# Kernel optimization log

Measured on AMD Instinct MI355X. Metric: run time of the kernel, lower is better.

The kernel has to match this reference:

```python
import jax, jax.numpy as jnp
import numpy as np

N = 16384   # total nodes (16 graphs x 32x32 grid)
E = 65536   # edges (before self loops)
F_IN = 7
H = 8       # gat heads
C = 200     # gat hidden per head
HC = H * C  # 1600
GCN = 1600
CNN = 64
OUT = 6
B = 16      # graphs per batch
G = 32      # grid size
EPS = 1e-5


def _bn1(x, g, b):
    # BatchNorm1d, training-mode batch stats (biased var), x: [N, F]
    mu = x.mean(0)
    var = x.var(0)
    return (x - mu) * jax.lax.rsqrt(var + EPS) * g + b


def _bn2(x, g, b):
    # BatchNorm2d over (N, H, W), x: [B, C, H, W]
    mu = x.mean((0, 2, 3), keepdims=True)
    var = x.var((0, 2, 3), keepdims=True)
    return (x - mu) * jax.lax.rsqrt(var + EPS) * g[None, :, None, None] + b[None, :, None, None]


def _conv5(x, w, b):
    y = jax.lax.conv_general_dilated(x, w, (1, 1), [(2, 2), (2, 2)],
                                     dimension_numbers=('NCHW', 'OIHW', 'NCHW'))
    return y + b[None, :, None, None]


def _gatv2(x, Wl, bl, Wr, br, We, att, bias, src, dst, edge_attr):
    # PyG GATv2Conv: concat=True, add_self_loops=True (fill_value='mean'), edge_dim=1
    n = x.shape[0]
    xl = (x @ Wl + bl).reshape(n, H, C)  # source transform
    xr = (x @ Wr + br).reshape(n, H, C)  # target transform
    loop = jnp.arange(n, dtype=src.dtype)
    s = jnp.concatenate([src, loop])
    d = jnp.concatenate([dst, loop])
    ea_loop = jnp.broadcast_to(edge_attr.mean(0, keepdims=True), (n, edge_attr.shape[1]))
    ea = jnp.concatenate([edge_attr, ea_loop], 0)
    ee = (ea @ We).reshape(-1, H, C)
    m = jax.nn.leaky_relu(xl[s] + xr[d] + ee, 0.2)       # [E+N, H, C]
    alpha = jnp.einsum('ehc,hc->eh', m, att)             # [E+N, H]
    amax = jax.ops.segment_max(alpha, d, num_segments=n)
    ex = jnp.exp(alpha - amax[d])
    denom = jax.ops.segment_sum(ex, d, num_segments=n)
    a = ex / denom[d]                                    # scatter-softmax over in-edges
    out = jax.ops.segment_sum(xl[s] * a[:, :, None], d, num_segments=n)  # [N, H, C]
    return out.reshape(n, HC) + bias


def setup_inputs() -> dict:
    k = jax.random.key(0)
    ks = jax.random.split(k, 16)
    def nrm(i, shape, s):
        return jax.random.normal(ks[i], shape, jnp.float32) * s
    z = lambda *s: jnp.zeros(s, jnp.float32)
    o = lambda *s: jnp.ones(s, jnp.float32)
    return {
        'x': nrm(0, (N, F_IN), 1.0),
        'edge_attr': jax.random.uniform(ks[1], (E, 1), jnp.float32),
        'Wl': nrm(2, (F_IN, HC), 0.3), 'bl': z(HC),
        'Wr': nrm(3, (F_IN, HC), 0.3), 'br': z(HC),
        'We': nrm(4, (1, HC), 0.3), 'att': nrm(5, (H, C), 0.1), 'gat_b': z(HC),
        'bn1_g': o(HC), 'bn1_b': z(HC),
        'W1': nrm(6, (HC, GCN), 0.025), 'b1': z(GCN),
        'bn2_g': o(GCN), 'bn2_b': z(GCN),
        'W2': nrm(7, (GCN, GCN), 0.025), 'b2': z(GCN),
        'Wp': nrm(8, (GCN, CNN), 0.025), 'bp': z(CNN),
        'cw1': nrm(9, (CNN, CNN, 5, 5), 0.025), 'cb1': z(CNN), 'g1': o(CNN), 'be1': z(CNN),
        'cw2': nrm(10, (128, CNN, 5, 5), 0.025), 'cb2': z(128), 'g2': o(128), 'be2': z(128),
        'cw3': nrm(11, (CNN, 128, 5, 5), 0.025), 'cb3': z(CNN), 'g3': o(CNN), 'be3': z(CNN),
        'cw4': nrm(12, (OUT, CNN, 5, 5), 0.025), 'cb4': z(OUT),
        'src': jax.random.randint(ks[13], (E,), 0, N, jnp.int32),
        'dst': jax.random.randint(ks[14], (E,), 0, N, jnp.int32),
    }


def reference(x, edge_attr, Wl, bl, Wr, br, We, att, gat_b, bn1_g, bn1_b,
              W1, b1, bn2_g, bn2_b, W2, b2, Wp, bp,
              cw1, cb1, g1, be1, cw2, cb2, g2, be2, cw3, cb3, g3, be3, cw4, cb4,
              src, dst):
    h = _gatv2(x, Wl, bl, Wr, br, We, att, gat_b, src, dst, edge_attr)
    h = jax.nn.leaky_relu(_bn1(h, bn1_g, bn1_b), 0.01)
    h = jax.nn.relu(_bn1(h @ W1 + b1, bn2_g, bn2_b))
    h = jax.nn.relu(h @ W2 + b2)
    # per-graph projection + reshape to grid (batch vector is contiguous arange//1024)
    h = (h @ Wp + bp).reshape(B, G, G, CNN).transpose(0, 3, 1, 2)  # [B, CNN, G, G]
    h = jax.nn.relu(_bn2(_conv5(h, cw1, cb1), g1, be1))
    h = jax.nn.relu(_bn2(_conv5(h, cw2, cb2), g2, be2))
    h = jax.nn.relu(_bn2(_conv5(h, cw3, cb3), g3, be3))
    return _conv5(h, cw4, cb4)  # [B, 6, G, G]
```

## Files before the change

kernel.cpp:

```cpp
#include <hip/hip_runtime.h>
#include <cstdint>
#include <cstddef>

#define N_NODES 16384
#define N_EDGES 65536
#define EN_TOT  (N_EDGES + N_NODES)
#define FIN 7
#define HC 1600
#define NH 8
#define CHD 200
#define GCN 1600
#define CNN 64
#define BATCH 16
#define BN_EPS 1e-5f

typedef unsigned short ushort_t;
typedef __attribute__((ext_vector_type(8))) short s8frag;
typedef __attribute__((ext_vector_type(4))) float f32x4;

__device__ __forceinline__ ushort_t f2bf(float f) {
    unsigned u = __float_as_uint(f);
    unsigned r = (u + 0x7FFFu + ((u >> 16) & 1u)) >> 16;
    return (ushort_t)r;
}
__device__ __forceinline__ float bf2f(ushort_t u) {
    return __uint_as_float(((unsigned)u) << 16);
}

__device__ __forceinline__ void gload16(const void* g, void* l) {
    __builtin_amdgcn_global_load_lds((const __attribute__((address_space(1))) void*)g,
                                     (__attribute__((address_space(3))) void*)l, 16, 0, 0);
}

#define SWZ_KOFF(tid) ((((tid) & 3) ^ (((tid) >> 3) & 3)) << 3)
#define SWZ_AQ(lane, am) (((((lane) >> 4) ^ (((am) >> 1) & 3)) << 3))

__global__ __launch_bounds__(256) void k_count(
    const int* __restrict__ dst, const float* __restrict__ ea,
    int* __restrict__ cnt, float* __restrict__ ea_sum)
{
    int e = blockIdx.x * 256 + threadIdx.x;
    int d = (e < N_EDGES) ? dst[e] : (e - N_EDGES);
    atomicAdd(&cnt[d], 1);
    float v = (e < N_EDGES) ? ea[e] : 0.f;
#pragma unroll
    for (int o = 1; o < 64; o <<= 1) v += __shfl_xor(v, o);
    if ((threadIdx.x & 63) == 0) atomicAdd(ea_sum, v);
}

__global__ __launch_bounds__(256) void k_scan(int* __restrict__ cnt, int* __restrict__ offs)
{
    __shared__ int part[256];
    int t = threadIdx.x;
    int base_i = t * 64;
    int s = 0;
    for (int i = 0; i < 64; i++) s += cnt[base_i + i];
    part[t] = s;
    __syncthreads();
    for (int o = 1; o < 256; o <<= 1) {
        int add = (t >= o) ? part[t - o] : 0;
        __syncthreads();
        part[t] += add;
        __syncthreads();
    }
    int run = (t == 0) ? 0 : part[t - 1];
    for (int i = 0; i < 64; i++) {
        int v = cnt[base_i + i];
        offs[base_i + i] = run;
        run += v;
        cnt[base_i + i] = 0;
    }
    if (t == 255) offs[N_NODES] = run;
}

__global__ __launch_bounds__(256) void k_fill(const int* __restrict__ dst,
    const int* __restrict__ offs, int* __restrict__ cur, int* __restrict__ eid)
{
    int e = blockIdx.x * 256 + threadIdx.x;
    if (e >= EN_TOT) return;
    int d = (e < N_EDGES) ? dst[e] : (e - N_EDGES);
    int pos = offs[d] + atomicAdd(&cur[d], 1);
    eid[pos] = e;
}

__global__ __launch_bounds__(256) void k_gprep(
    const float* __restrict__ Wl, const float* __restrict__ bl,
    const float* __restrict__ Wr, const float* __restrict__ br,
    const float* __restrict__ We, const float* __restrict__ att,
    ushort_t* __restrict__ G, float* __restrict__ att16)
{
    int cp = blockIdx.x * 256 + threadIdx.x;
    if (cp >= 8 * 208) return;
    int h = cp / 208, j = cp - h * 208;
    ushort_t v[32];
#pragma unroll
    for (int k = 0; k < 32; k++) v[k] = 0;
    float av = 0.f;
    if (j < 200) {
        int c = h * 200 + j;
#pragma unroll
        for (int k = 0; k < 7; k++) v[k]     = f2bf(Wl[k * HC + c]);
#pragma unroll
        for (int k = 0; k < 7; k++) v[7 + k] = f2bf(Wr[k * HC + c]);
        v[14] = f2bf(We[c]);
        v[15] = f2bf(bl[c] + br[c]);
        av = att[h * CHD + j];
    }
    uint4* dst4 = (uint4*)(G + (size_t)cp * 32);
#pragma unroll
    for (int i = 0; i < 4; i++) dst4[i] = ((uint4*)v)[i];
    att16[cp] = av;
}

__global__ __launch_bounds__(256) void k_alpha_mm(
    const float* __restrict__ x, const float* __restrict__ edge_attr,
    const float* __restrict__ ea_sum, const int* __restrict__ src,
    const int* __restrict__ dst, const ushort_t* __restrict__ G,
    const float* __restrict__ att16, float* __restrict__ alpha)
{
    __shared__ ushort_t Fs[64 * 32];
    int tid = threadIdx.x;
    int lane = tid & 63, w = tid >> 6;
    int e0 = blockIdx.x * 64;
    float eam = ea_sum[0] * (1.f / (float)N_EDGES);

#define FSLOT(j, k) ((j) * 32 + ((((k) >> 3) ^ (((j) >> 1) & 3)) << 3) + ((k) & 7))
    for (int i = tid; i < 64 * 16; i += 256) {
        int j = i >> 4, k = (i & 15) + 16;
        Fs[FSLOT(j, k)] = 0;
    }
    {
        int j = tid >> 2, part = tid & 3;
        int e = e0 + j;
        int s, d; float ea;
        if (e < N_EDGES) { s = src[e]; d = dst[e]; ea = edge_attr[e]; }
        else             { s = e - N_EDGES; d = s; ea = eam; }
        if (part == 0) {
#pragma unroll
            for (int k = 0; k < 4; k++) Fs[FSLOT(j, k)] = f2bf(x[s * 7 + k]);
        } else if (part == 1) {
#pragma unroll
            for (int k = 4; k < 7; k++) Fs[FSLOT(j, k)] = f2bf(x[s * 7 + k]);
            Fs[FSLOT(j, 7)] = f2bf(x[d * 7 + 0]);
        } else if (part == 2) {
#pragma unroll
            for (int k = 1; k < 5; k++) Fs[FSLOT(j, 7 + k)] = f2bf(x[d * 7 + k]);
        } else {
            Fs[FSLOT(j, 12)] = f2bf(x[d * 7 + 5]);
            Fs[FSLOT(j, 13)] = f2bf(x[d * 7 + 6]);
            Fs[FSLOT(j, 14)] = f2bf(ea);
            Fs[FSLOT(j, 15)] = f2bf(1.0f);
        }
    }
#undef FSLOT
    __syncthreads();

    int am = lane & 15;
    int aq = (lane >> 4) * 8;
    s8frag afrag = *(const s8frag*)&Fs[(w * 16 + am) * 32 + SWZ_AQ(lane, am)];
    int lr4 = (lane >> 4) * 4;
    int ew = e0 + w * 16;
#pragma unroll
    for (int h = 0; h < NH; h++) {
        f32x4 hacc = (f32x4)0.f;
        int colbase = h * 208;
#pragma unroll
        for (int t = 0; t < 13; t++) {
            int cb = colbase + t * 16;
            s8frag bfrag = *(const s8frag*)(G + ((size_t)(cb + am) * 32 + aq));
            f32x4 z = (f32x4)0.f;
            f32x4 p = __builtin_amdgcn_mfma_f32_16x16x32_bf16(afrag, bfrag, z, 0, 0, 0);
            float attv = att16[cb + am];
#pragma unroll
            for (int r = 0; r < 4; r++) {
                float v = p[r];
                v = (v >= 0.f) ? v : 0.2f * v;
                hacc[r] += v * attv;
            }
        }
#pragma unroll
        for (int o = 1; o <= 8; o <<= 1) {
#pragma unroll
            for (int r = 0; r < 4; r++) hacc[r] += __shfl_xor(hacc[r], o);
        }
        if (am == 0) {
#pragma unroll
            for (int r = 0; r < 4; r++)
                alpha[(size_t)(ew + lr4 + r) * NH + h] = hacc[r];
        }
    }
}

__global__ __launch_bounds__(256) void k_agg_x(
    const float* __restrict__ x, const float* __restrict__ alpha,
    const int* __restrict__ offs, const int* __restrict__ eid,
    const int* __restrict__ src, float* __restrict__ xbar)
{
    int n = blockIdx.x * 4 + (threadIdx.x >> 6);
    int lane = threadIdx.x & 63;
    int beg = offs[n], deg = offs[n + 1] - beg;

    float pm[NH];
#pragma unroll
    for (int h = 0; h < NH; h++) pm[h] = -1e30f;
    for (int j = lane; j < deg; j += 64) {
        int e = eid[beg + j];
        const float* ap = alpha + (size_t)e * NH;
#pragma unroll
        for (int h = 0; h < NH; h++) pm[h] = fmaxf(pm[h], ap[h]);
    }
#pragma unroll
    for (int h = 0; h < NH; h++)
#pragma unroll
        for (int o = 1; o < 64; o <<= 1)
            pm[h] = fmaxf(pm[h], __shfl_xor(pm[h], o));

    float ps[NH];
    float px[NH][7];
#pragma unroll
    for (int h = 0; h < NH; h++) {
        ps[h] = 0.f;
#pragma unroll
        for (int k = 0; k < 7; k++) px[h][k] = 0.f;
    }
    for (int j = lane; j < deg; j += 64) {
        int e = eid[beg + j];
        int s = (e < N_EDGES) ? src[e] : (e - N_EDGES);
        float xv[7];
#pragma unroll
        for (int k = 0; k < 7; k++) xv[k] = x[s * 7 + k];
        const float* ap = alpha + (size_t)e * NH;
#pragma unroll
        for (int h = 0; h < NH; h++) {
            float p = __expf(ap[h] - pm[h]);
            ps[h] += p;
#pragma unroll
            for (int k = 0; k < 7; k++) px[h][k] += p * xv[k];
        }
    }
#pragma unroll
    for (int h = 0; h < NH; h++) {
#pragma unroll
        for (int o = 1; o < 64; o <<= 1) ps[h] += __shfl_xor(ps[h], o);
#pragma unroll
        for (int k = 0; k < 7; k++)
#pragma unroll
            for (int o = 1; o < 64; o <<= 1) px[h][k] += __shfl_xor(px[h][k], o);
    }
    float val = 0.f;
#pragma unroll
    for (int h = 0; h < NH; h++)
#pragma unroll
        for (int k = 0; k < 7; k++)
            if (lane == h * 7 + k) val = px[h][k] / ps[h];
    if (lane < 56) xbar[(size_t)n * 56 + lane] = val;
}

__global__ __launch_bounds__(256) void k_xmom(
    const float* __restrict__ xbar, float* __restrict__ mom)
{
    int h = blockIdx.x & 7, chunk = blockIdx.x >> 3;
    int tid = threadIdx.x, lane = tid & 63;
    float mu[7], S[49];
#pragma unroll
    for (int k = 0; k < 7; k++) mu[k] = 0.f;
#pragma unroll
    for (int k = 0; k < 49; k++) S[k] = 0.f;
    for (int i = 0; i < 8; i++) {
        int n = chunk * 2048 + i * 256 + tid;
        const float* xb = xbar + (size_t)n * 56 + h * 7;
        float xv[7];
#pragma unroll
        for (int k = 0; k < 7; k++) xv[k] = xb[k];
#pragma unroll
        for (int k = 0; k < 7; k++) {
            mu[k] += xv[k];
#pragma unroll
            for (int kk = 0; kk < 7; kk++) S[k * 7 + kk] += xv[k] * xv[kk];
        }
    }
#pragma unroll
    for (int o = 1; o < 64; o <<= 1) {
#pragma unroll
        for (int k = 0; k < 7; k++) mu[k] += __shfl_xor(mu[k], o);
#pragma unroll
        for (int k = 0; k < 49; k++) S[k] += __shfl_xor(S[k], o);
    }
    if (lane == 0) {
        float* mh = mom + h * 56;
#pragma unroll
        for (int k = 0; k < 7; k++) atomicAdd(&mh[k], mu[k]);
#pragma unroll
        for (int k = 0; k < 49; k++) atomicAdd(&mh[7 + k], S[k]);
    }
}

__global__ __launch_bounds__(256) void k_bn1_prep(
    const float* __restrict__ mom, const float* __restrict__ Wl,
    const float* __restrict__ bl, const float* __restrict__ gat_b,
    const float* __restrict__ g, const float* __restrict__ b,
    float* __restrict__ scale, float* __restrict__ shift)
{
    int f = blockIdx.x * 256 + threadIdx.x;
    if (f >= HC) return;
    int h = f / CHD;
    const float* mh = mom + h * 56;
    const float inv = 1.f / (float)N_NODES;
    float m[7], w[7];
#pragma unroll
    for (int k = 0; k < 7; k++) {
        m[k] = mh[k] * inv;
        w[k] = Wl[k * HC + f];
    }
    float mean = bl[f] + gat_b[f];
#pragma unroll
    for (int k = 0; k < 7; k++) mean += w[k] * m[k];
    float var = 0.f;
#pragma unroll
    for (int k = 0; k < 7; k++)
#pragma unroll
        for (int kk = 0; kk < 7; kk++)
            var += w[k] * w[kk] * (mh[7 + k * 7 + kk] * inv - m[k] * m[kk]);
    var = fmaxf(var, 0.f);
    float sc = g[f] * rsqrtf(var + BN_EPS);
    scale[f] = sc;
    shift[f] = b[f] - mean * sc;
}

__global__ __launch_bounds__(256) void k_project_bn(
    const float* __restrict__ xbar, const float* __restrict__ Wl,
    const float* __restrict__ bl, const float* __restrict__ gat_b,
    const float* __restrict__ scale, const float* __restrict__ shift,
    ushort_t* __restrict__ hout)
{
    int idx = blockIdx.x * 256 + threadIdx.x;
    int n = idx / HC, f = idx - n * HC;
    int h = f / CHD;
    const float* xb = xbar + (size_t)n * 56 + h * 7;
    float s = bl[f] + gat_b[f];
#pragma unroll
    for (int k = 0; k < 7; k++) s += xb[k] * Wl[k * HC + f];
    float v = s * scale[f] + shift[f];
    v = (v >= 0.f) ? v : 0.01f * v;
    hout[idx] = f2bf(v);
}

__global__ __launch_bounds__(256) void k_bn_apply_bb(
    const ushort_t* __restrict__ X, ushort_t* __restrict__ Y,
    const float* __restrict__ bsum, const float* __restrict__ bsq,
    const float* __restrict__ g, const float* __restrict__ b,
    int rows, int total, int F)
{
    int idx = blockIdx.x * 256 + threadIdx.x;
    if (idx >= total) return;
    int f = idx % F;
    float inv = 1.f / (float)rows;
    float mu = bsum[f] * inv;
    float var = bsq[f] * inv - mu * mu;
    float sc = g[f] * rsqrtf(var + BN_EPS);
    float sh = b[f] - mu * sc;
    float v = bf2f(X[idx]) * sc + sh;
    v = fmaxf(v, 0.f);
    Y[idx] = f2bf(v);
}

__global__ __launch_bounds__(256) void k_bn_apply_pad(
    const ushort_t* __restrict__ X, ushort_t* __restrict__ pad,
    const float* __restrict__ bsum, const float* __restrict__ bsq,
    const float* __restrict__ g, const float* __restrict__ b,
    int total, int Csh)
{
    int idx = blockIdx.x * 256 + threadIdx.x;
    if (idx >= total) return;
    int C = 1 << Csh;
    int c = idx & (C - 1);
    int pix = idx >> Csh;
    int xx = pix & 31, yy = (pix >> 5) & 31, bb = pix >> 10;
    float inv = 1.f / 16384.f;
    float mu = bsum[c] * inv;
    float var = bsq[c] * inv - mu * mu;
    float sc = g[c] * rsqrtf(var + BN_EPS);
    float sh = b[c] - mu * sc;
    float v = bf2f(X[idx]) * sc + sh;
    v = fmaxf(v, 0.f);
    pad[((size_t)((bb * 36 + yy + 2) * 36 + xx + 2) << Csh) + c] = f2bf(v);
}

__global__ __launch_bounds__(256) void k_wt(
    const float* __restrict__ W, ushort_t* __restrict__ BT, int Kdim, int Ndim, int Npad)
{
    __shared__ float t[32][33];
    int tx = threadIdx.x & 31, ty = threadIdx.x >> 5;
    int n0 = blockIdx.x * 32, k0 = blockIdx.y * 32;
#pragma unroll
    for (int i = 0; i < 4; i++)
        t[ty + i * 8][tx] = (n0 + tx < Ndim)
            ? W[(size_t)(k0 + ty + i * 8) * Ndim + n0 + tx] : 0.f;
    __syncthreads();
#pragma unroll
    for (int i = 0; i < 4; i++)
        BT[(size_t)(n0 + ty + i * 8) * Kdim + k0 + tx] = f2bf(t[tx][ty + i * 8]);
}

__global__ __launch_bounds__(256) void k_cwt_all(
    const float* __restrict__ w1, const float* __restrict__ w2,
    const float* __restrict__ w3, const float* __restrict__ w4,
    ushort_t* __restrict__ o1, ushort_t* __restrict__ o2,
    ushort_t* __restrict__ o3, ushort_t* __restrict__ o4)
{
    int idx = blockIdx.x * 256 + threadIdx.x;
    const int R1 = 128 * 1600, R2 = 128 * 1600, R3 = 128 * 3200;
    const float* w; ushort_t* o; int local, K, Cin, Cout;
    if (idx < R1)                { w = w1; o = o1; local = idx; K = 1600; Cin = 64;  Cout = 64; }
    else if (idx < R1 + R2)      { w = w2; o = o2; local = idx - R1; K = 1600; Cin = 64; Cout = 128; }
    else if (idx < R1 + R2 + R3) { w = w3; o = o3; local = idx - R1 - R2; K = 3200; Cin = 128; Cout = 64; }
    else                         { w = w4; o = o4; local = idx - R1 - R2 - R3; K = 1600; Cin = 64; Cout = 6; }
    int co = local / K;
    int k = local - co * K;
    int p = k / Cin, ci = k - p * Cin;
    o[local] = (co < Cout) ? f2bf(w[(size_t)(co * Cin + ci) * 25 + p]) : (ushort_t)0;
}

__global__ __launch_bounds__(256) void k_mgemm(
    const ushort_t* __restrict__ A, const ushort_t* __restrict__ BT,
    const float* __restrict__ bias, ushort_t* __restrict__ Cb,
    float* __restrict__ bsum, float* __restrict__ bsq,
    int K, int Nvalid, int ldc, int relu)
{
    __shared__ __align__(16) ushort_t As[128 * 32];
    __shared__ __align__(16) ushort_t Bs[128 * 32];
    int tid = threadIdx.x;
    int lane = tid & 63;
    int wid = tid >> 6;
    int wy = wid >> 1, wx = wid & 1;

    int nx = gridDim.x;
    int lin = blockIdx.y * nx + blockIdx.x;
    int xcd = lin & 7;
    int q = lin >> 3;
    int colb = q % nx;
    int rowb = (q / nx) * 8 + xcd;
    int row0 = rowb * 128, col0 = colb * 128;

    f32x4 acc[4][4];
#pragma unroll
    for (int i = 0; i < 4; i++)
#pragma unroll
        for (int j = 0; j < 4; j++) acc[i][j] = (f32x4)0.f;

    int rA = tid >> 2;
    int koff = SWZ_KOFF(tid);
    const ushort_t* Ag = A + (size_t)row0 * K + koff;
    const ushort_t* Bg = BT + (size_t)col0 * K + koff;

    int am = lane & 15;
    int swz = SWZ_AQ(lane, am);
    int aoff0 = (wy * 64 + am) * 32 + swz;
    int boff0 = (wx * 64 + am) * 32 + swz;

    for (int kk = 0; kk < K; kk += 32) {
        __syncthreads();
        gload16(Ag + (size_t)rA * K + kk,        (char*)As + tid * 16);
        gload16(Ag + (size_t)(rA + 64) * K + kk, (char*)As + (tid + 256) * 16);
        gload16(Bg + (size_t)rA * K + kk,        (char*)Bs + tid * 16);
        gload16(Bg + (size_t)(rA + 64) * K + kk, (char*)Bs + (tid + 256) * 16);
        __syncthreads();

        s8frag a[4], b[4];
#pragma unroll
        for (int mi = 0; mi < 4; mi++)
            a[mi] = *(const s8frag*)&As[aoff0 + mi * 16 * 32];
#pragma unroll
        for (int ni = 0; ni < 4; ni++)
            b[ni] = *(const s8frag*)&Bs[boff0 + ni * 16 * 32];
#pragma unroll
        for (int mi = 0; mi < 4; mi++)
#pragma unroll
            for (int ni = 0; ni < 4; ni++)
                acc[mi][ni] = __builtin_amdgcn_mfma_f32_16x16x32_bf16(
                    a[mi], b[ni], acc[mi][ni], 0, 0, 0);
    }

    int lc = lane & 15, lr4 = (lane >> 4) * 4;
#pragma unroll
    for (int ni = 0; ni < 4; ni++) {
        int col = col0 + wx * 64 + ni * 16 + lc;
        bool valid = col < Nvalid;
        float bv = valid ? bias[col] : 0.f;
        float s = 0.f, q2 = 0.f;
#pragma unroll
        for (int mi = 0; mi < 4; mi++) {
#pragma unroll
            for (int r = 0; r < 4; r++) {
                int row = row0 + wy * 64 + mi * 16 + lr4 + r;
                float v = acc[mi][ni][r] + bv;
                s += v; q2 += v * v;
                float vo = relu ? fmaxf(v, 0.f) : v;
                if (valid) Cb[(size_t)row * ldc + col] = f2bf(vo);
            }
        }
        if (bsum != nullptr && valid) {
            s += __shfl_xor(s, 16);  s += __shfl_xor(s, 32);
            q2 += __shfl_xor(q2, 16); q2 += __shfl_xor(q2, 32);
            if ((lane >> 4) == 0) {
                atomicAdd(&bsum[col], s);
                atomicAdd(&bsq[col], q2);
            }
        }
    }
}

__global__ __launch_bounds__(256) void k_cgemm3(
    const ushort_t* __restrict__ Ain, const ushort_t* __restrict__ BT,
    const float* __restrict__ bias, float* __restrict__ Cf, ushort_t* __restrict__ Cb,
    float* __restrict__ bsum, float* __restrict__ bsq,
    int K, int Csh, int Nvalid, int ldc, int out_mode, int linA)
{
    __shared__ __align__(16) ushort_t As[32 * 32];
    __shared__ __align__(16) ushort_t Bs[64 * 32];
    int tid = threadIdx.x;
    int lane = tid & 63;
    int w = tid >> 6, wr = w >> 1, wc = w & 1;
    int row0 = blockIdx.y * 32, col0 = blockIdx.x * 64;
    int Cmask = (1 << Csh) - 1;

    f32x4 acc[2];
    acc[0] = (f32x4)0.f; acc[1] = (f32x4)0.f;

    int rB = tid >> 2;
    int koffB = SWZ_KOFF(tid);
    const ushort_t* Bg = BT + (size_t)(col0 + rB) * K + koffB;

    int rA = (tid & 127) >> 2;
    int koffA = SWZ_KOFF(tid & 127);
    int pix0 = row0 + rA;
    int b0 = pix0 >> 10, y0 = (pix0 >> 5) & 31, x0 = pix0 & 31;

    int am = lane & 15;
    int swz = SWZ_AQ(lane, am);

    for (int kk = 0; kk < K; kk += 32) {
        __syncthreads();
        if (tid < 128) {
            if (linA) {
                gload16(Ain + (size_t)(row0 + rA) * K + kk + koffA, (char*)As + tid * 16);
            } else {
                int k = kk + koffA;
                int p = k >> Csh;
                int ci = k & Cmask;
                int ky = p / 5, kx = p - ky * 5;
                gload16(Ain + (((size_t)((b0 * 36 + y0 + ky) * 36 + x0 + kx) << Csh) + ci),
                        (char*)As + tid * 16);
            }
        }
        gload16(Bg + kk, (char*)Bs + tid * 16);
        __syncthreads();

        s8frag a = *(const s8frag*)&As[(wr * 16 + am) * 32 + swz];
        s8frag b0f = *(const s8frag*)&Bs[(wc * 32 + am) * 32 + swz];
        s8frag b1f = *(const s8frag*)&Bs[(wc * 32 + 16 + am) * 32 + swz];
        acc[0] = __builtin_amdgcn_mfma_f32_16x16x32_bf16(a, b0f, acc[0], 0, 0, 0);
        acc[1] = __builtin_amdgcn_mfma_f32_16x16x32_bf16(a, b1f, acc[1], 0, 0, 0);
    }

    int lc = lane & 15, lr4 = (lane >> 4) * 4;
#pragma unroll
    for (int ni = 0; ni < 2; ni++) {
        int col = col0 + wc * 32 + ni * 16 + lc;
        bool valid = col < Nvalid;
        float bv = valid ? bias[col] : 0.f;
        float s = 0.f, q2 = 0.f;
#pragma unroll
        for (int r = 0; r < 4; r++) {
            int row = row0 + wr * 16 + lr4 + r;
            float v = acc[ni][r] + bv;
            s += v; q2 += v * v;
            if (valid) {
                if (out_mode == 1) {
                    Cb[(size_t)row * ldc + col] = f2bf(v);
                } else if (out_mode == 3) {
                    int bb = row >> 10, sp = row & 1023;
                    int yy = sp >> 5, xx = sp & 31;
                    Cb[((size_t)((bb * 36 + yy + 2) * 36 + xx + 2) << 6) + col] = f2bf(v);
                } else {
                    int bb = row >> 10, sp = row & 1023;
                    Cf[(size_t)((bb * 6 + col) << 10) + sp] = v;
                }
            }
        }
        if (bsum != nullptr && valid) {
            s += __shfl_xor(s, 16);  s += __shfl_xor(s, 32);
            q2 += __shfl_xor(q2, 16); q2 += __shfl_xor(q2, 32);
            if ((lane >> 4) == 0) {
                atomicAdd(&bsum[col], s);
                atomicAdd(&bsq[col], q2);
            }
        }
    }
}

extern "C" void kernel_launch(void* const* d_in, const int* in_sizes, int n_in,
                              void* d_out, int out_size, void* d_ws, size_t ws_size,
                              hipStream_t stream)
{
    const float* x   = (const float*)d_in[0];
    const float* ea  = (const float*)d_in[1];
    const float* Wl  = (const float*)d_in[2];
    const float* bl  = (const float*)d_in[3];
    const float* Wr  = (const float*)d_in[4];
    const float* br  = (const float*)d_in[5];
    const float* We  = (const float*)d_in[6];
    const float* att = (const float*)d_in[7];
    const float* gat_b = (const float*)d_in[8];
    const float* bn1_g = (const float*)d_in[9];
    const float* bn1_b = (const float*)d_in[10];
    const float* W1 = (const float*)d_in[11];
    const float* b1 = (const float*)d_in[12];
    const float* bn2_g = (const float*)d_in[13];
    const float* bn2_b = (const float*)d_in[14];
    const float* W2 = (const float*)d_in[15];
    const float* b2 = (const float*)d_in[16];
    const float* Wp = (const float*)d_in[17];
    const float* bp = (const float*)d_in[18];
    const float* cw1 = (const float*)d_in[19]; const float* cb1 = (const float*)d_in[20];
    const float* g1  = (const float*)d_in[21]; const float* be1 = (const float*)d_in[22];
    const float* cw2 = (const float*)d_in[23]; const float* cb2 = (const float*)d_in[24];
    const float* g2  = (const float*)d_in[25]; const float* be2 = (const float*)d_in[26];
    const float* cw3 = (const float*)d_in[27]; const float* cb3 = (const float*)d_in[28];
    const float* g3  = (const float*)d_in[29]; const float* be3 = (const float*)d_in[30];
    const float* cw4 = (const float*)d_in[31]; const float* cb4 = (const float*)d_in[32];
    const int* src = (const int*)d_in[33];
    const int* dst = (const int*)d_in[34];
    float* out = (float*)d_out;

    const size_t SZ_REGION = (size_t)N_NODES * HC * 4;
    const size_t HALF = SZ_REGION / 2;
    char* ws = (char*)d_ws;
    char* regA = ws;
    char* regB = regA + SZ_REGION;
    char* wbase = regB + SZ_REGION;
    ushort_t* W1T  = (ushort_t*)wbase;
    ushort_t* W2T  = W1T + (size_t)1664 * 1600;
    ushort_t* WpT  = W2T + (size_t)1664 * 1600;
    ushort_t* c1T  = WpT + (size_t)128 * 1600;
    ushort_t* c2T  = c1T + (size_t)128 * 1600;
    ushort_t* c3T  = c2T + (size_t)128 * 1600;
    ushort_t* c4T  = c3T + (size_t)128 * 3200;
    ushort_t* G16  = c4T + (size_t)128 * 1600;
    float* att16   = (float*)(G16 + (size_t)1664 * 32);
    float* alpha   = att16 + 1664 + 64;
    float* xbar    = alpha + (size_t)EN_TOT * NH;
    float* bn_sc   = xbar + (size_t)N_NODES * 56;
    float* bn_sh   = bn_sc + HC;
    int*   cnt    = (int*)(bn_sh + HC + 64);
    float* ea_sum = (float*)(cnt + N_NODES);
    float* mom    = ea_sum + 16;
    float* bnG1   = mom + 448;
    float* bnC1   = bnG1 + 3200;
    float* bnC2   = bnC1 + 256;
    float* bnC3   = bnC2 + 256;
    const size_t ZBYTES = (char*)(bnC3 + 256) - (char*)cnt;
    int* offs = (int*)(bnC3 + 256 + 16);
    int* eid  = offs + N_NODES + 1 + 63;

    ushort_t* abuf16  = (ushort_t*)regA;
    ushort_t* a2buf16 = (ushort_t*)(regA + HALF);
    ushort_t* pad1 = (ushort_t*)regA;
    ushort_t* pad2 = (ushort_t*)(regA + (4u << 20));
    ushort_t* pad3 = (ushort_t*)(regA + (8u << 20));
    ushort_t* pad4 = (ushort_t*)(regA + (14u << 20));
    ushort_t* c1out = (ushort_t*)(regA + (18u << 20));
    ushort_t* c2out = (ushort_t*)(regA + (22u << 20));
    ushort_t* c3out = (ushort_t*)(regA + (27u << 20));
    ushort_t* g1b16   = (ushort_t*)regB;
    ushort_t* h3_16   = (ushort_t*)regB;

    k_wt<<<dim3(52, 50), 256, 0, stream>>>(W1, W1T, 1600, 1600, 1664);
    k_wt<<<dim3(52, 50), 256, 0, stream>>>(W2, W2T, 1600, 1600, 1664);
    k_wt<<<dim3(4, 50), 256, 0, stream>>>(Wp, WpT, 1600, 64, 128);
    k_cwt_all<<<4000, 256, 0, stream>>>(cw1, cw2, cw3, cw4, c1T, c2T, c3T, c4T);
    k_gprep<<<7, 256, 0, stream>>>(Wl, bl, Wr, br, We, att, G16, att16);

    hipMemsetAsync(cnt, 0, ZBYTES, stream);
    k_count<<<EN_TOT / 256, 256, 0, stream>>>(dst, ea, cnt, ea_sum);
    k_scan<<<1, 256, 0, stream>>>(cnt, offs);
    k_fill<<<EN_TOT / 256, 256, 0, stream>>>(dst, offs, cnt, eid);
    k_alpha_mm<<<EN_TOT / 64, 256, 0, stream>>>(x, ea, ea_sum, src, dst, G16, att16, alpha);
    k_agg_x<<<N_NODES / 4, 256, 0, stream>>>(x, alpha, offs, eid, src, xbar);

    k_xmom<<<64, 256, 0, stream>>>(xbar, mom);
    k_bn1_prep<<<7, 256, 0, stream>>>(mom, Wl, bl, gat_b, bn1_g, bn1_b, bn_sc, bn_sh);
    k_project_bn<<<(N_NODES * HC) / 256, 256, 0, stream>>>(xbar, Wl, bl, gat_b, bn_sc, bn_sh, abuf16);

    k_mgemm<<<dim3(13, 128), 256, 0, stream>>>(abuf16, W1T, b1, g1b16,
                                               bnG1, bnG1 + 1600, 1600, 1600, 1600, 0);
    k_bn_apply_bb<<<(N_NODES * GCN) / 256, 256, 0, stream>>>(g1b16, a2buf16,
                                                             bnG1, bnG1 + 1600, bn2_g, bn2_b,
                                                             N_NODES, N_NODES * GCN, GCN);
    k_mgemm<<<dim3(13, 128), 256, 0, stream>>>(a2buf16, W2T, b2, h3_16,
                                               (float*)nullptr, (float*)nullptr, 1600, 1600, 1600, 1);

    hipMemsetAsync(regA, 0, (size_t)17 << 20, stream);

    k_cgemm3<<<dim3(1, 512), 256, 0, stream>>>(h3_16, WpT, bp, (float*)nullptr, pad1,
                                               (float*)nullptr, (float*)nullptr,
                                               1600, 6, 64, 64, 3, 1);
    k_cgemm3<<<dim3(1, 512), 256, 0, stream>>>(pad1, c1T, cb1, (float*)nullptr, c1out,
                                               bnC1, bnC1 + 128, 1600, 6, 64, 64, 1, 0);
    k_bn_apply_pad<<<(16384 * 64) / 256, 256, 0, stream>>>(c1out, pad2, bnC1, bnC1 + 128,
                                                           g1, be1, 16384 * 64, 6);
    k_cgemm3<<<dim3(2, 512), 256, 0, stream>>>(pad2, c2T, cb2, (float*)nullptr, c2out,
                                               bnC2, bnC2 + 128, 1600, 6, 128, 128, 1, 0);
    k_bn_apply_pad<<<(16384 * 128) / 256, 256, 0, stream>>>(c2out, pad3, bnC2, bnC2 + 128,
                                                            g2, be2, 16384 * 128, 7);
    k_cgemm3<<<dim3(1, 512), 256, 0, stream>>>(pad3, c3T, cb3, (float*)nullptr, c3out,
                                               bnC3, bnC3 + 128, 3200, 7, 64, 64, 1, 0);
    k_bn_apply_pad<<<(16384 * 64) / 256, 256, 0, stream>>>(c3out, pad4, bnC3, bnC3 + 128,
                                                           g3, be3, 16384 * 64, 6);
    k_cgemm3<<<dim3(1, 512), 256, 0, stream>>>(pad4, c4T, cb4, out, (ushort_t*)nullptr,
                                               (float*)nullptr, (float*)nullptr,
                                               1600, 6, 6, 6, 2, 0);

    (void)in_sizes; (void)n_in; (void)out_size; (void)ws_size;
}
```

Baseline: 917.1 us.

## Vectorize elementwise BN kernels and double K-step in dense MFMA GEMM

The projection+BN kernel now uses one block per node, with xbar staged in shared memory and each thread handling 8 features through float4 loads and a single 16-byte store. The two BN-apply kernels likewise process 8 bf16 elements per thread with 16-byte loads and stores. The dense GEMM moves from a 32 to a 64 K-slice per LDS stage with an XOR swizzle, halving barrier count per K at the cost of double the shared memory. That larger LDS footprint may reduce occupancy, and the vector accesses assume feature counts divisible by 8.

```diff
diff --git a/kernel.cpp b/kernel.cpp
--- a/kernel.cpp
+++ b/kernel.cpp
@@ -333,57 +333,109 @@
     const float* __restrict__ scale, const float* __restrict__ shift,
     ushort_t* __restrict__ hout)
 {
-    int idx = blockIdx.x * 256 + threadIdx.x;
-    int n = idx / HC, f = idx - n * HC;
-    int h = f / CHD;
-    const float* xb = xbar + (size_t)n * 56 + h * 7;
-    float s = bl[f] + gat_b[f];
-#pragma unroll
-    for (int k = 0; k < 7; k++) s += xb[k] * Wl[k * HC + f];
-    float v = s * scale[f] + shift[f];
-    v = (v >= 0.f) ? v : 0.01f * v;
-    hout[idx] = f2bf(v);
+    __shared__ float xs[56];
+    int n = blockIdx.x, tid = threadIdx.x;
+    if (tid < 56) xs[tid] = xbar[(size_t)n * 56 + tid];
+    __syncthreads();
+    if (tid >= 200) return;
+    int f0 = tid * 8;
+    int h = f0 / CHD;
+    float xb[7];
+#pragma unroll
+    for (int k = 0; k < 7; k++) xb[k] = xs[h * 7 + k];
+    float acc[8];
+    {
+        float4 b0 = *(const float4*)(bl + f0), b1 = *(const float4*)(bl + f0 + 4);
+        float4 g0 = *(const float4*)(gat_b + f0), g1 = *(const float4*)(gat_b + f0 + 4);
+        acc[0] = b0.x + g0.x; acc[1] = b0.y + g0.y; acc[2] = b0.z + g0.z; acc[3] = b0.w + g0.w;
+        acc[4] = b1.x + g1.x; acc[5] = b1.y + g1.y; acc[6] = b1.z + g1.z; acc[7] = b1.w + g1.w;
+    }
+#pragma unroll
+    for (int k = 0; k < 7; k++) {
+        float4 w0 = *(const float4*)(Wl + k * HC + f0);
+        float4 w1 = *(const float4*)(Wl + k * HC + f0 + 4);
+        acc[0] += xb[k] * w0.x; acc[1] += xb[k] * w0.y;
+        acc[2] += xb[k] * w0.z; acc[3] += xb[k] * w0.w;
+        acc[4] += xb[k] * w1.x; acc[5] += xb[k] * w1.y;
+        acc[6] += xb[k] * w1.z; acc[7] += xb[k] * w1.w;
+    }
+    float4 s0 = *(const float4*)(scale + f0), s1 = *(const float4*)(scale + f0 + 4);
+    float4 h0 = *(const float4*)(shift + f0), h1 = *(const float4*)(shift + f0 + 4);
+    float sc[8] = {s0.x, s0.y, s0.z, s0.w, s1.x, s1.y, s1.z, s1.w};
+    float sh[8] = {h0.x, h0.y, h0.z, h0.w, h1.x, h1.y, h1.z, h1.w};
+    ushort_t o[8];
+#pragma unroll
+    for (int i = 0; i < 8; i++) {
+        float v = acc[i] * sc[i] + sh[i];
+        v = (v >= 0.f) ? v : 0.01f * v;
+        o[i] = f2bf(v);
+    }
+    *(uint4*)(hout + (size_t)n * HC + f0) = *(uint4*)o;
 }
 
 __global__ __launch_bounds__(256) void k_bn_apply_bb(
     const ushort_t* __restrict__ X, ushort_t* __restrict__ Y,
     const float* __restrict__ bsum, const float* __restrict__ bsq,
     const float* __restrict__ g, const float* __restrict__ b,
-    int rows, int total, int F)
+    int rows, int total8, int F)
 {
     int idx = blockIdx.x * 256 + threadIdx.x;
-    if (idx >= total) return;
-    int f = idx % F;
+    if (idx >= total8) return;
+    int e0 = idx * 8;
+    int f0 = e0 % F;
     float inv = 1.f / (float)rows;
-    float mu = bsum[f] * inv;
-    float var = bsq[f] * inv - mu * mu;
-    float sc = g[f] * rsqrtf(var + BN_EPS);
-    float sh = b[f] - mu * sc;
-    float v = bf2f(X[idx]) * sc + sh;
-    v = fmaxf(v, 0.f);
-    Y[idx] = f2bf(v);
+    uint4 xin = *(const uint4*)(X + e0);
+    ushort_t* xv = (ushort_t*)&xin;
+    ushort_t o[8];
+#pragma unroll
+    for (int i = 0; i < 8; i += 4) {
+        float4 su = *(const float4*)(bsum + f0 + i);
+        float4 sq = *(const float4*)(bsq + f0 + i);
+        float4 gg = *(const float4*)(g + f0 + i);
+        float4 bb = *(const float4*)(b + f0 + i);
+        float mu, var, sc, sh, v;
+#define DO1(comp, j) \
+        mu = su.comp * inv; var = sq.comp * inv - mu * mu; \
+        sc = gg.comp * rsqrtf(var + BN_EPS); sh = bb.comp - mu * sc; \
+        v = bf2f(xv[i + j]) * sc + sh; v = fmaxf(v, 0.f); o[i + j] = f2bf(v);
+        DO1(x, 0) DO1(y, 1) DO1(z, 2) DO1(w, 3)
+#undef DO1
+    }
+    *(uint4*)(Y + e0) = *(uint4*)o;
 }
 
 __global__ __launch_bounds__(256) void k_bn_apply_pad(
     const ushort_t* __restrict__ X, ushort_t* __restrict__ pad,
     const float* __restrict__ bsum, const float* __restrict__ bsq,
     const float* __restrict__ g, const float* __restrict__ b,
-    int total, int Csh)
+    int total8, int Csh)
 {
     int idx = blockIdx.x * 256 + threadIdx.x;
-    if (idx >= total) return;
+    if (idx >= total8) return;
+    int e0 = idx * 8;
     int C = 1 << Csh;
-    int c = idx & (C - 1);
-    int pix = idx >> Csh;
-    int xx = pix & 31, yy = (pix >> 5) & 31, bb = pix >> 10;
+    int c0 = e0 & (C - 1);
+    int pix = e0 >> Csh;
+    int xx = pix & 31, yy = (pix >> 5) & 31, bb2 = pix >> 10;
     float inv = 1.f / 16384.f;
-    float mu = bsum[c] * inv;
-    float var = bsq[c] * inv - mu * mu;
-    float sc = g[c] * rsqrtf(var + BN_EPS);
-    float sh = b[c] - mu * sc;
-    float v = bf2f(X[idx]) * sc + sh;
-    v = fmaxf(v, 0.f);
-    pad[((size_t)((bb * 36 + yy + 2) * 36 + xx + 2) << Csh) + c] = f2bf(v);
+    uint4 xin = *(const uint4*)(X + e0);
+    ushort_t* xv = (ushort_t*)&xin;
+    ushort_t o[8];
+#pragma unroll
+    for (int i = 0; i < 8; i += 4) {
+        float4 su = *(const float4*)(bsum + c0 + i);
+        float4 sq = *(const float4*)(bsq + c0 + i);
+        float4 gg = *(const float4*)(g + c0 + i);
+        float4 bb = *(const float4*)(b + c0 + i);
+        float mu, var, sc, sh, v;
+#define DO1(comp, j) \
+        mu = su.comp * inv; var = sq.comp * inv - mu * mu; \
+        sc = gg.comp * rsqrtf(var + BN_EPS); sh = bb.comp - mu * sc; \
+        v = bf2f(xv[i + j]) * sc + sh; v = fmaxf(v, 0.f); o[i + j] = f2bf(v);
+        DO1(x, 0) DO1(y, 1) DO1(z, 2) DO1(w, 3)
+#undef DO1
+    }
+    *(uint4*)(pad + (((size_t)((bb2 * 36 + yy + 2) * 36 + xx + 2)) << Csh) + c0) = *(uint4*)o;
 }
 
 __global__ __launch_bounds__(256) void k_wt(
@@ -427,8 +479,8 @@
     float* __restrict__ bsum, float* __restrict__ bsq,
     int K, int Nvalid, int ldc, int relu)
 {
-    __shared__ __align__(16) ushort_t As[128 * 32];
-    __shared__ __align__(16) ushort_t Bs[128 * 32];
+    __shared__ __align__(16) ushort_t As[128 * 64];
+    __shared__ __align__(16) ushort_t Bs[128 * 64];
     int tid = threadIdx.x;
     int lane = tid & 63;
     int wid = tid >> 6;
@@ -448,40 +500,41 @@
 #pragma unroll
         for (int j = 0; j < 4; j++) acc[i][j] = (f32x4)0.f;
 
-    int rA = tid >> 2;
-    int koff = SWZ_KOFF(tid);
-    const ushort_t* Ag = A + (size_t)row0 * K + koff;
-    const ushort_t* Bg = BT + (size_t)col0 * K + koff;
-
-    int am = lane & 15;
-    int swz = SWZ_AQ(lane, am);
-    int aoff0 = (wy * 64 + am) * 32 + swz;
-    int boff0 = (wx * 64 + am) * 32 + swz;
-
-    for (int kk = 0; kk < K; kk += 32) {
+    int am = lane & 15, qq = lane >> 4;
+    int lr4 = qq * 4;
+
+    for (int kk = 0; kk < K; kk += 64) {
         __syncthreads();
-        gload16(Ag + (size_t)rA * K + kk,        (char*)As + tid * 16);
-        gload16(Ag + (size_t)(rA + 64) * K + kk, (char*)As + (tid + 256) * 16);
-        gload16(Bg + (size_t)rA * K + kk,        (char*)Bs + tid * 16);
-        gload16(Bg + (size_t)(rA + 64) * K + kk, (char*)Bs + (tid + 256) * 16);
+#pragma unroll
+        for (int j = 0; j < 4; j++) {
+            int sA = j * 256 + tid;
+            int rowS = sA >> 3, cS = sA & 7;
+            int srcC = (cS ^ (rowS & 7)) << 3;
+            gload16(A  + (size_t)(row0 + rowS) * K + kk + srcC, (char*)As + sA * 16);
+            gload16(BT + (size_t)(col0 + rowS) * K + kk + srcC, (char*)Bs + sA * 16);
+        }
         __syncthreads();
 
-        s8frag a[4], b[4];
-#pragma unroll
-        for (int mi = 0; mi < 4; mi++)
-            a[mi] = *(const s8frag*)&As[aoff0 + mi * 16 * 32];
-#pragma unroll
-        for (int ni = 0; ni < 4; ni++)
-            b[ni] = *(const s8frag*)&Bs[boff0 + ni * 16 * 32];
-#pragma unroll
-        for (int mi = 0; mi < 4; mi++)
+#pragma unroll
+        for (int t = 0; t < 2; t++) {
+            int sw = ((((t << 2) | qq) ^ (am & 7)) << 3);
+            s8frag a[4], b[4];
+#pragma unroll
+            for (int mi = 0; mi < 4; mi++)
+                a[mi] = *(const s8frag*)&As[(wy * 64 + mi * 16 + am) * 64 + sw];
 #pragma unroll
             for (int ni = 0; ni < 4; ni++)
-                acc[mi][ni] = __builtin_amdgcn_mfma_f32_16x16x32_bf16(
-                    a[mi], b[ni], acc[mi][ni], 0, 0, 0);
-    }
-
-    int lc = lane & 15, lr4 = (lane >> 4) * 4;
+                b[ni] = *(const s8frag*)&Bs[(wx * 64 + ni * 16 + am) * 64 + sw];
+#pragma unroll
+            for (int mi = 0; mi < 4; mi++)
+#pragma unroll
+                for (int ni = 0; ni < 4; ni++)
+                    acc[mi][ni] = __builtin_amdgcn_mfma_f32_16x16x32_bf16(
+                        a[mi], b[ni], acc[mi][ni], 0, 0, 0);
+        }
+    }
+
+    int lc = am;
 #pragma unroll
     for (int ni = 0; ni < 4; ni++) {
         int col = col0 + wx * 64 + ni * 16 + lc;
@@ -502,7 +555,7 @@
         if (bsum != nullptr && valid) {
             s += __shfl_xor(s, 16);  s += __shfl_xor(s, 32);
             q2 += __shfl_xor(q2, 16); q2 += __shfl_xor(q2, 32);
-            if ((lane >> 4) == 0) {
+            if (qq == 0) {
                 atomicAdd(&bsum[col], s);
                 atomicAdd(&bsq[col], q2);
             }
@@ -690,13 +743,13 @@
 
     k_xmom<<<64, 256, 0, stream>>>(xbar, mom);
     k_bn1_prep<<<7, 256, 0, stream>>>(mom, Wl, bl, gat_b, bn1_g, bn1_b, bn_sc, bn_sh);
-    k_project_bn<<<(N_NODES * HC) / 256, 256, 0, stream>>>(xbar, Wl, bl, gat_b, bn_sc, bn_sh, abuf16);
+    k_project_bn<<<N_NODES, 256, 0, stream>>>(xbar, Wl, bl, gat_b, bn_sc, bn_sh, abuf16);
 
     k_mgemm<<<dim3(13, 128), 256, 0, stream>>>(abuf16, W1T, b1, g1b16,
                                                bnG1, bnG1 + 1600, 1600, 1600, 1600, 0);
-    k_bn_apply_bb<<<(N_NODES * GCN) / 256, 256, 0, stream>>>(g1b16, a2buf16,
-                                                             bnG1, bnG1 + 1600, bn2_g, bn2_b,
-                                                             N_NODES, N_NODES * GCN, GCN);
+    k_bn_apply_bb<<<(N_NODES * GCN / 8) / 256, 256, 0, stream>>>(g1b16, a2buf16,
+                                                                 bnG1, bnG1 + 1600, bn2_g, bn2_b,
+                                                                 N_NODES, N_NODES * GCN / 8, GCN);
     k_mgemm<<<dim3(13, 128), 256, 0, stream>>>(a2buf16, W2T, b2, h3_16,
                                                (float*)nullptr, (float*)nullptr, 1600, 1600, 1600, 1);
 
@@ -707,16 +760,16 @@
                                                1600, 6, 64, 64, 3, 1);
     k_cgemm3<<<dim3(1, 512), 256, 0, stream>>>(pad1, c1T, cb1, (float*)nullptr, c1out,
                                                bnC1, bnC1 + 128, 1600, 6, 64, 64, 1, 0);
-    k_bn_apply_pad<<<(16384 * 64) / 256, 256, 0, stream>>>(c1out, pad2, bnC1, bnC1 + 128,
-                                                           g1, be1, 16384 * 64, 6);
+    k_bn_apply_pad<<<(16384 * 64 / 8) / 256, 256, 0, stream>>>(c1out, pad2, bnC1, bnC1 + 128,
+                                                               g1, be1, 16384 * 64 / 8, 6);
     k_cgemm3<<<dim3(2, 512), 256, 0, stream>>>(pad2, c2T, cb2, (float*)nullptr, c2out,
                                                bnC2, bnC2 + 128, 1600, 6, 128, 128, 1, 0);
-    k_bn_apply_pad<<<(16384 * 128) / 256, 256, 0, stream>>>(c2out, pad3, bnC2, bnC2 + 128,
-                                                            g2, be2, 16384 * 128, 7);
+    k_bn_apply_pad<<<(16384 * 128 / 8) / 256, 256, 0, stream>>>(c2out, pad3, bnC2, bnC2 + 128,
+                                                                g2, be2, 16384 * 128 / 8, 7);
     k_cgemm3<<<dim3(1, 512), 256, 0, stream>>>(pad3, c3T, cb3, (float*)nullptr, c3out,
                                                bnC3, bnC3 + 128, 3200, 7, 64, 64, 1, 0);
-    k_bn_apply_pad<<<(16384 * 64) / 256, 256, 0, stream>>>(c3out, pad4, bnC3, bnC3 + 128,
-                                                           g3, be3, 16384 * 64, 6);
+    k_bn_apply_pad<<<(16384 * 64 / 8) / 256, 256, 0, stream>>>(c3out, pad4, bnC3, bnC3 + 128,
+                                                               g3, be3, 16384 * 64 / 8, 6);
     k_cgemm3<<<dim3(1, 512), 256, 0, stream>>>(pad4, c4T, cb4, out, (ushort_t*)nullptr,
                                                (float*)nullptr, (float*)nullptr,
                                                1600, 6, 6, 6, 2, 0);
```

Result: faster. 867.1 us (-5.5%).
